# Kernel tuning notes

Hardware: AMD Instinct MI355X
Metric: run time of the kernel (lower is better)

The kernel has to match this reference:

```python
import jax, jax.numpy as jnp
import numpy as np

def setup_inputs() -> dict:
    key = jax.random.key(0)
    k1, k2, k3 = jax.random.split(key, 3)
    N_net, d, n_t, n_in = 1, 4, 2048, 256
    n_h, n = 8, 256
    STD = 0.02  # E_std / Q_std in the original init
    r_prime = jax.random.normal(k1, (N_net, d, n_t, n_in), dtype=jnp.float32)
    Q = STD * jax.random.normal(k2, (N_net, n_h, n_in, n_in), dtype=jnp.float32)
    E = STD * jax.random.normal(k3, (N_net, n_h, n, n_in), dtype=jnp.float32)
    return {"r_prime": r_prime, "Q": Q, "E": E}

def reference(r_prime, Q, E):
    # r_prime: [N, b, t, i_in]; Q: [N, h, i_in, j_in]; E: [N, h, n, j_in]
    n_t = r_prime.shape[2]
    # Omega[N,b,h,t,u] = r_t^T Q^h r_u  (bilinear attention scores, no softmax)
    Omega = jnp.einsum('Nbti,Nhij,Nbuj->Nbhtu', r_prime, Q, r_prime)
    # Causal mask (lower-triangular Theta), applied inside the second contraction.
    Theta = jnp.tril(jnp.ones((n_t, n_t), dtype=r_prime.dtype))
    # r[N,b,t,i_out] = sum_{u<=t,h} Omega[t,u] * (E^h r_u)_i
    r = jnp.einsum('Nbhtu,tu,Nhij,Nbuj->Nbti', Omega, Theta, E, r_prime)
    return r
```

## Files before the change

### kernel.cpp

```cpp
#include <hip/hip_runtime.h>

typedef __attribute__((ext_vector_type(4))) float f32x4;
typedef __attribute__((ext_vector_type(8))) short s16x8;

#define DEVI static __device__ __forceinline__

constexpr int BB = 4, HH = 8, TT = 2048, DD = 256;

DEVI short f2bf(float f) {
  union { float f; unsigned u; } x; x.f = f;
  unsigned r = x.u + 0x7fffu + ((x.u >> 16) & 1u);
  return (short)(r >> 16);
}

__global__ void cast_prep(const float* __restrict__ r, const float* __restrict__ Q,
                          const float* __restrict__ E,
                          short* __restrict__ rbf, short* __restrict__ Qt,
                          short* __restrict__ Ebf) {
  int idx = blockIdx.x * blockDim.x + threadIdx.x;
  int stride = gridDim.x * blockDim.x;
  for (int i = idx; i < BB * TT * DD; i += stride) rbf[i] = f2bf(r[i]);
  for (int i = idx; i < HH * DD * DD; i += stride) {
    int h = i / (DD * DD), rem = i % (DD * DD), j = rem / DD, i2 = rem % DD;
    Qt[i] = f2bf(Q[(h * DD + i2) * DD + j]);
    Ebf[i] = f2bf(E[i]);
  }
}

__global__ __launch_bounds__(256, 2)
void prep_gemm(const short* __restrict__ rbf, const short* __restrict__ Qt,
               const short* __restrict__ Ebf, short* __restrict__ Abf,
               short* __restrict__ Vtbf, int mode) {
  __shared__ __align__(16) short w_lds[64 * 256];
  int tid = threadIdx.x, lane = tid & 63, wid = tid >> 6;
  int h = blockIdx.y, b = blockIdx.z, bx = blockIdx.x;
  const short* X; const short* W; short* C; int ldC, m0, n0;
  if (mode == 0) {
    m0 = (bx >> 2) * 64; n0 = (bx & 3) * 64;
    X = rbf + (size_t)b * TT * DD;
    W = Qt + (size_t)h * DD * DD;
    C = Abf + (size_t)(b * HH + h) * TT * DD; ldC = DD;
  } else {
    m0 = (bx & 3) * 64; n0 = (bx >> 2) * 64;
    X = Ebf + (size_t)h * DD * DD;
    W = rbf + (size_t)b * TT * DD;
    C = Vtbf + (size_t)(b * HH + h) * DD * TT; ldC = TT;
  }
  #pragma unroll
  for (int it = 0; it < 8; ++it) {
    int t = it * 256 + tid;
    int row = t >> 5, kb = t & 31;
    s16x8 v = *(const s16x8*)(W + (size_t)(n0 + row) * DD + kb * 8);
    *(s16x8*)(&w_lds[row * 256 + ((kb ^ (row & 7)) << 3)]) = v;
  }
  s16x8 a[8];
  {
    const short* xrow = X + (size_t)(m0 + wid * 16 + (lane & 15)) * DD + (lane >> 4) * 8;
    #pragma unroll
    for (int ks = 0; ks < 8; ++ks) a[ks] = *(const s16x8*)(xrow + ks * 32);
  }
  __syncthreads();
  f32x4 c[4] = {};
  #pragma unroll
  for (int n = 0; n < 4; ++n) {
    int row = n * 16 + (lane & 15);
    #pragma unroll
    for (int ks = 0; ks < 8; ++ks) {
      int kb = ks * 4 + (lane >> 4);
      s16x8 bfr = *(const s16x8*)(&w_lds[row * 256 + ((kb ^ (row & 7)) << 3)]);
      c[n] = __builtin_amdgcn_mfma_f32_16x16x32_bf16(a[ks], bfr, c[n], 0, 0, 0);
    }
  }
  #pragma unroll
  for (int n = 0; n < 4; ++n) {
    int col = n0 + n * 16 + (lane & 15);
    #pragma unroll
    for (int rr = 0; rr < 4; ++rr) {
      int row = m0 + wid * 16 + (lane >> 4) * 4 + rr;
      C[(size_t)row * ldC + col] = f2bf(c[n][rr]);
    }
  }
}

__global__ __launch_bounds__(256, 2)
void attn_main(const short* __restrict__ Abf, const short* __restrict__ Kbf,
               const short* __restrict__ Vtb, float* __restrict__ out) {
  __shared__ __align__(16) short k_lds[64 * 256];
  __shared__ __align__(16) short v_lds[256 * 64];
  __shared__ __align__(16) short s_lds[64 * 64];
  int tid = threadIdx.x, lane = tid & 63, wid = tid >> 6;
  int t0 = blockIdx.x * 64, h = blockIdx.y, b = blockIdx.z;

  const short* Ab = Abf + ((size_t)(b * HH + h) * TT + t0) * DD;
  const short* Kb = Kbf + (size_t)b * TT * DD;
  const short* Vb = Vtb + (size_t)(b * HH + h) * DD * TT;

  s16x8 a[8];
  {
    const short* arow = Ab + (size_t)(wid * 16 + (lane & 15)) * DD + (lane >> 4) * 8;
    #pragma unroll
    for (int ks = 0; ks < 8; ++ks) a[ks] = *(const s16x8*)(arow + ks * 32);
  }
  f32x4 acc[16] = {};

  int nU = t0 / 64 + 1;
  for (int iu = 0; iu < nU; ++iu) {
    int U = iu * 64;
    __syncthreads();
    {
      const short* src = Kb + (size_t)U * DD;
      #pragma unroll
      for (int it = 0; it < 8; ++it) {
        int t = it * 256 + tid;
        int row = t >> 5, kb = t & 31;
        s16x8 v = *(const s16x8*)(src + (size_t)row * DD + kb * 8);
        *(s16x8*)(&k_lds[row * 256 + ((kb ^ (row & 7)) << 3)]) = v;
      }
      const short* vsrc = Vb + U;
      #pragma unroll
      for (int it = 0; it < 8; ++it) {
        int t = it * 256 + tid;
        int row = t >> 3, cb = t & 7;
        s16x8 v = *(const s16x8*)(vsrc + (size_t)row * TT + cb * 8);
        *(s16x8*)(&v_lds[row * 64 + ((cb ^ (row & 7)) << 3)]) = v;
      }
    }
    __syncthreads();

    f32x4 s[4] = {};
    #pragma unroll
    for (int n = 0; n < 4; ++n) {
      int row = n * 16 + (lane & 15);
      #pragma unroll
      for (int ks = 0; ks < 8; ++ks) {
        int kb = ks * 4 + (lane >> 4);
        s16x8 bfr = *(const s16x8*)(&k_lds[row * 256 + ((kb ^ (row & 7)) << 3)]);
        s[n] = __builtin_amdgcn_mfma_f32_16x16x32_bf16(a[ks], bfr, s[n], 0, 0, 0);
      }
    }
    int trow_base = t0 + wid * 16 + (lane >> 4) * 4;
    #pragma unroll
    for (int n = 0; n < 4; ++n) {
      int u_col = U + n * 16 + (lane & 15);
      #pragma unroll
      for (int rr = 0; rr < 4; ++rr) {
        float v = (u_col <= trow_base + rr) ? s[n][rr] : 0.0f;
        int srow = (lane >> 4) * 4 + rr;
        int scol = n * 16 + (lane & 15);
        s_lds[(wid * 16 + srow) * 64 + (((scol >> 3) ^ (srow & 7)) << 3) + (scol & 7)] = f2bf(v);
      }
    }

    #pragma unroll
    for (int ks = 0; ks < 2; ++ks) {
      int srow = lane & 15;
      int kb = ks * 4 + (lane >> 4);
      s16x8 af = *(const s16x8*)(&s_lds[(wid * 16 + srow) * 64 + ((kb ^ (srow & 7)) << 3)]);
      #pragma unroll
      for (int ni = 0; ni < 16; ++ni) {
        int vrow = ni * 16 + (lane & 15);
        s16x8 bfr = *(const s16x8*)(&v_lds[vrow * 64 + ((kb ^ (vrow & 7)) << 3)]);
        acc[ni] = __builtin_amdgcn_mfma_f32_16x16x32_bf16(af, bfr, acc[ni], 0, 0, 0);
      }
    }
  }

  float* ob = out + ((size_t)b * TT + t0 + wid * 16) * DD;
  #pragma unroll
  for (int ni = 0; ni < 16; ++ni) {
    int col = ni * 16 + (lane & 15);
    #pragma unroll
    for (int rr = 0; rr < 4; ++rr) {
      int row = (lane >> 4) * 4 + rr;
      atomicAdd(&ob[row * DD + col], acc[ni][rr]);
    }
  }
}

extern "C" void kernel_launch(void* const* d_in, const int* in_sizes, int n_in,
                              void* d_out, int out_size, void* d_ws, size_t ws_size,
                              hipStream_t stream) {
  const float* r = (const float*)d_in[0];
  const float* Q = (const float*)d_in[1];
  const float* E = (const float*)d_in[2];
  float* out = (float*)d_out;
  char* ws = (char*)d_ws;

  size_t off = 0;
  short* rbf = (short*)(ws + off); off += (size_t)BB * TT * DD * 2;
  short* Qt  = (short*)(ws + off); off += (size_t)HH * DD * DD * 2;
  short* Ebf = (short*)(ws + off); off += (size_t)HH * DD * DD * 2;
  short* Abf = (short*)(ws + off); off += (size_t)BB * HH * TT * DD * 2;
  short* Vtb = (short*)(ws + off); off += (size_t)BB * HH * DD * TT * 2;

  hipMemsetAsync(d_out, 0, (size_t)out_size * sizeof(float), stream);
  cast_prep<<<1024, 256, 0, stream>>>(r, Q, E, rbf, Qt, Ebf);
  prep_gemm<<<dim3(128, HH, BB), 256, 0, stream>>>(rbf, Qt, Ebf, Abf, Vtb, 0);
  prep_gemm<<<dim3(128, HH, BB), 256, 0, stream>>>(rbf, Qt, Ebf, Abf, Vtb, 1);
  attn_main<<<dim3(TT / 64, HH, BB), 256, 0, stream>>>(Abf, rbf, Vtb, out);
}
```

Baseline: 266.7 us.

## Restructure causal attention with 128-row tiles, paired load balancing, and direct-to-LDS loads

The main kernel now processes 128 query rows per block instead of 64, pairing tile p with tile 15-p so every block does the same amount of causal work. Key blocks are split between two blocks by parity, and their partial sums are combined with the existing atomics. K and V tiles are loaded with global_load_lds straight into swizzled LDS, skipping the register round trip. prep_gemm now stages its output through LDS so the global stores are coalesced 16-byte writes. Each wave now holds more accumulator registers (32 f32x4), which risks lower occupancy or spills, and the grid is smaller (16x8x4 blocks).

```diff
diff --git a/kernel.cpp b/kernel.cpp
--- a/kernel.cpp
+++ b/kernel.cpp
@@ -11,6 +11,12 @@
   union { float f; unsigned u; } x; x.f = f;
   unsigned r = x.u + 0x7fffu + ((x.u >> 16) & 1u);
   return (short)(r >> 16);
+}
+
+DEVI void gl16(const short* g, short* l) {
+  __builtin_amdgcn_global_load_lds(
+      (const __attribute__((address_space(1))) void*)g,
+      (__attribute__((address_space(3))) void*)l, 16, 0, 0);
 }
 
 __global__ void cast_prep(const float* __restrict__ r, const float* __restrict__ Q,
@@ -71,14 +77,24 @@
       c[n] = __builtin_amdgcn_mfma_f32_16x16x32_bf16(a[ks], bfr, c[n], 0, 0, 0);
     }
   }
+  __syncthreads();
   #pragma unroll
   for (int n = 0; n < 4; ++n) {
-    int col = n0 + n * 16 + (lane & 15);
+    int col = n * 16 + (lane & 15);
+    int cb = col >> 3;
     #pragma unroll
     for (int rr = 0; rr < 4; ++rr) {
-      int row = m0 + wid * 16 + (lane >> 4) * 4 + rr;
-      C[(size_t)row * ldC + col] = f2bf(c[n][rr]);
-    }
+      int row = wid * 16 + (lane >> 4) * 4 + rr;
+      w_lds[row * 64 + ((cb ^ (row & 7)) << 3) + (col & 7)] = f2bf(c[n][rr]);
+    }
+  }
+  __syncthreads();
+  #pragma unroll
+  for (int q = 0; q < 2; ++q) {
+    int t = q * 256 + tid;
+    int row = t >> 3, cb = t & 7;
+    s16x8 v = *(const s16x8*)(&w_lds[row * 64 + ((cb ^ (row & 7)) << 3)]);
+    *(s16x8*)(&C[(size_t)(m0 + row) * ldC + n0 + cb * 8]) = v;
   }
 }
 
@@ -87,92 +103,111 @@
                const short* __restrict__ Vtb, float* __restrict__ out) {
   __shared__ __align__(16) short k_lds[64 * 256];
   __shared__ __align__(16) short v_lds[256 * 64];
-  __shared__ __align__(16) short s_lds[64 * 64];
+  __shared__ __align__(16) short s_lds[128 * 32];
   int tid = threadIdx.x, lane = tid & 63, wid = tid >> 6;
-  int t0 = blockIdx.x * 64, h = blockIdx.y, b = blockIdx.z;
-
-  const short* Ab = Abf + ((size_t)(b * HH + h) * TT + t0) * DD;
+  int pp = blockIdx.x;
+  int p = pp >> 1, par = pp & 1;
+  int h = blockIdx.y, b = blockIdx.z;
+
+  const short* Ab0 = Abf + (size_t)(b * HH + h) * TT * DD;
   const short* Kb = Kbf + (size_t)b * TT * DD;
   const short* Vb = Vtb + (size_t)(b * HH + h) * DD * TT;
 
-  s16x8 a[8];
-  {
-    const short* arow = Ab + (size_t)(wid * 16 + (lane & 15)) * DD + (lane >> 4) * 8;
-    #pragma unroll
-    for (int ks = 0; ks < 8; ++ks) a[ks] = *(const s16x8*)(arow + ks * 32);
-  }
-  f32x4 acc[16] = {};
-
-  int nU = t0 / 64 + 1;
-  for (int iu = 0; iu < nU; ++iu) {
-    int U = iu * 64;
-    __syncthreads();
+  #pragma unroll 1
+  for (int hv = 0; hv < 2; ++hv) {
+    int tt = hv ? (15 - p) : p;
+    s16x8 a[2][8];
     {
-      const short* src = Kb + (size_t)U * DD;
+      const short* abase = Ab0 + (size_t)(tt * 128 + wid * 32 + (lane & 15)) * DD + ((lane >> 4) << 3);
       #pragma unroll
-      for (int it = 0; it < 8; ++it) {
-        int t = it * 256 + tid;
-        int row = t >> 5, kb = t & 31;
-        s16x8 v = *(const s16x8*)(src + (size_t)row * DD + kb * 8);
-        *(s16x8*)(&k_lds[row * 256 + ((kb ^ (row & 7)) << 3)]) = v;
+      for (int rb = 0; rb < 2; ++rb)
+        #pragma unroll
+        for (int ks = 0; ks < 8; ++ks)
+          a[rb][ks] = *(const s16x8*)(abase + rb * 16 * DD + ks * 32);
+    }
+    f32x4 acc[2][16] = {};
+    int nU = 2 * tt + 2;
+    #pragma unroll 1
+    for (int iu = par; iu < nU; iu += 2) {
+      int U = iu * 64;
+      __syncthreads();
+      {
+        const short* ksrc = Kb + (size_t)U * DD;
+        #pragma unroll
+        for (int c = 0; c < 8; ++c) {
+          int kc = wid * 8 + c;
+          int row = kc * 2 + (lane >> 5);
+          int blk = lane & 31;
+          gl16(ksrc + (size_t)row * DD + ((blk ^ (row & 7)) << 3), &k_lds[kc * 512]);
+        }
+        #pragma unroll
+        for (int c = 0; c < 8; ++c) {
+          int vc = wid * 8 + c;
+          int row = vc * 8 + (lane >> 3);
+          int cb = lane & 7;
+          gl16(Vb + (size_t)row * TT + U + ((cb ^ (row & 7)) << 3), &v_lds[vc * 512]);
+        }
       }
-      const short* vsrc = Vb + U;
+      __syncthreads();
+
       #pragma unroll
-      for (int it = 0; it < 8; ++it) {
-        int t = it * 256 + tid;
-        int row = t >> 3, cb = t & 7;
-        s16x8 v = *(const s16x8*)(vsrc + (size_t)row * TT + cb * 8);
-        *(s16x8*)(&v_lds[row * 64 + ((cb ^ (row & 7)) << 3)]) = v;
+      for (int hh = 0; hh < 2; ++hh) {
+        f32x4 s[2][2] = {{{0,0,0,0},{0,0,0,0}},{{0,0,0,0},{0,0,0,0}}};
+        #pragma unroll
+        for (int n2 = 0; n2 < 2; ++n2) {
+          int row = (hh * 2 + n2) * 16 + (lane & 15);
+          #pragma unroll
+          for (int ks = 0; ks < 8; ++ks) {
+            int kb = ks * 4 + (lane >> 4);
+            s16x8 bfr = *(const s16x8*)(&k_lds[row * 256 + ((kb ^ (row & 7)) << 3)]);
+            s[0][n2] = __builtin_amdgcn_mfma_f32_16x16x32_bf16(a[0][ks], bfr, s[0][n2], 0, 0, 0);
+            s[1][n2] = __builtin_amdgcn_mfma_f32_16x16x32_bf16(a[1][ks], bfr, s[1][n2], 0, 0, 0);
+          }
+        }
+        #pragma unroll
+        for (int rb = 0; rb < 2; ++rb) {
+          #pragma unroll
+          for (int n2 = 0; n2 < 2; ++n2) {
+            #pragma unroll
+            for (int rr = 0; rr < 4; ++rr) {
+              int t_loc = wid * 32 + rb * 16 + (lane >> 4) * 4 + rr;
+              int u_glob = U + (hh * 2 + n2) * 16 + (lane & 15);
+              float v = (u_glob <= tt * 128 + t_loc) ? s[rb][n2][rr] : 0.0f;
+              int kloc = n2 * 16 + (lane & 15);
+              int cb = kloc >> 3;
+              s_lds[t_loc * 32 + ((cb ^ ((t_loc >> 1) & 3)) << 3) + (kloc & 7)] = f2bf(v);
+            }
+          }
+        }
+        s16x8 af[2];
+        #pragma unroll
+        for (int rb = 0; rb < 2; ++rb) {
+          int R = wid * 32 + rb * 16 + (lane & 15);
+          int cb2 = (lane >> 4) ^ ((R >> 1) & 3);
+          af[rb] = *(const s16x8*)(&s_lds[R * 32 + (cb2 << 3)]);
+        }
+        #pragma unroll
+        for (int ni = 0; ni < 16; ++ni) {
+          int vrow = ni * 16 + (lane & 15);
+          int ub = hh * 4 + (lane >> 4);
+          s16x8 bv = *(const s16x8*)(&v_lds[vrow * 64 + ((ub ^ (vrow & 7)) << 3)]);
+          acc[0][ni] = __builtin_amdgcn_mfma_f32_16x16x32_bf16(af[0], bv, acc[0][ni], 0, 0, 0);
+          acc[1][ni] = __builtin_amdgcn_mfma_f32_16x16x32_bf16(af[1], bv, acc[1][ni], 0, 0, 0);
+        }
       }
     }
-    __syncthreads();
-
-    f32x4 s[4] = {};
-    #pragma unroll
-    for (int n = 0; n < 4; ++n) {
-      int row = n * 16 + (lane & 15);
-      #pragma unroll
-      for (int ks = 0; ks < 8; ++ks) {
-        int kb = ks * 4 + (lane >> 4);
-        s16x8 bfr = *(const s16x8*)(&k_lds[row * 256 + ((kb ^ (row & 7)) << 3)]);
-        s[n] = __builtin_amdgcn_mfma_f32_16x16x32_bf16(a[ks], bfr, s[n], 0, 0, 0);
-      }
-    }
-    int trow_base = t0 + wid * 16 + (lane >> 4) * 4;
-    #pragma unroll
-    for (int n = 0; n < 4; ++n) {
-      int u_col = U + n * 16 + (lane & 15);
-      #pragma unroll
-      for (int rr = 0; rr < 4; ++rr) {
-        float v = (u_col <= trow_base + rr) ? s[n][rr] : 0.0f;
-        int srow = (lane >> 4) * 4 + rr;
-        int scol = n * 16 + (lane & 15);
-        s_lds[(wid * 16 + srow) * 64 + (((scol >> 3) ^ (srow & 7)) << 3) + (scol & 7)] = f2bf(v);
-      }
-    }
-
-    #pragma unroll
-    for (int ks = 0; ks < 2; ++ks) {
-      int srow = lane & 15;
-      int kb = ks * 4 + (lane >> 4);
-      s16x8 af = *(const s16x8*)(&s_lds[(wid * 16 + srow) * 64 + ((kb ^ (srow & 7)) << 3)]);
+    float* ob = out + ((size_t)b * TT + tt * 128 + wid * 32) * DD;
+    #pragma unroll
+    for (int rb = 0; rb < 2; ++rb) {
       #pragma unroll
       for (int ni = 0; ni < 16; ++ni) {
-        int vrow = ni * 16 + (lane & 15);
-        s16x8 bfr = *(const s16x8*)(&v_lds[vrow * 64 + ((kb ^ (vrow & 7)) << 3)]);
-        acc[ni] = __builtin_amdgcn_mfma_f32_16x16x32_bf16(af, bfr, acc[ni], 0, 0, 0);
+        int col = ni * 16 + (lane & 15);
+        #pragma unroll
+        for (int rr = 0; rr < 4; ++rr) {
+          int row = rb * 16 + (lane >> 4) * 4 + rr;
+          atomicAdd(&ob[row * DD + col], acc[rb][ni][rr]);
+        }
       }
-    }
-  }
-
-  float* ob = out + ((size_t)b * TT + t0 + wid * 16) * DD;
-  #pragma unroll
-  for (int ni = 0; ni < 16; ++ni) {
-    int col = ni * 16 + (lane & 15);
-    #pragma unroll
-    for (int rr = 0; rr < 4; ++rr) {
-      int row = (lane >> 4) * 4 + rr;
-      atomicAdd(&ob[row * DD + col], acc[ni][rr]);
     }
   }
 }
@@ -197,5 +232,5 @@
   cast_prep<<<1024, 256, 0, stream>>>(r, Q, E, rbf, Qt, Ebf);
   prep_gemm<<<dim3(128, HH, BB), 256, 0, stream>>>(rbf, Qt, Ebf, Abf, Vtb, 0);
   prep_gemm<<<dim3(128, HH, BB), 256, 0, stream>>>(rbf, Qt, Ebf, Abf, Vtb, 1);
-  attn_main<<<dim3(TT / 64, HH, BB), 256, 0, stream>>>(Abf, rbf, Vtb, out);
-}
+  attn_main<<<dim3(16, HH, BB), 256, 0, stream>>>(Abf, rbf, Vtb, out);
+}
```

After: 611.5 us. 129% more time.
